# Kernel tuning notes

Hardware: AMD Instinct MI355X
Metric: run time of the kernel (lower is better)

Reference implementation:

```python
import jax, jax.numpy as jnp
import numpy as np

N = 50000      # nodes
E = 200000     # edges
IN = 768       # in_dim
HID = 256      # hidden_dim
OUT = 64       # out_dim
H = 4          # heads in conv1
R = 6          # n_relations
NEG = 0.2      # LeakyReLU negative slope (PyG default)
EPS = 1e-5     # LayerNorm eps


def layer_norm(h, g, b):
    mu = jnp.mean(h, axis=-1, keepdims=True)
    var = jnp.mean((h - mu) ** 2, axis=-1, keepdims=True)
    return (h - mu) * jax.lax.rsqrt(var + EPS) * g + b


def gat_layer(x, src, dst, W, a_src, a_dst, bias, heads, dh):
    # project: [N, heads, dh]
    h = (x @ W).reshape(-1, heads, dh)
    # per-node attention logits [N, heads]
    al_s = jnp.sum(h * a_src, axis=-1)
    al_d = jnp.sum(h * a_dst, axis=-1)
    # per-edge scores (edge j->i: source contributes al_s[j], target al_d[i])
    e = jax.nn.leaky_relu(al_s[src] + al_d[dst], NEG)  # [E, heads]
    # segment softmax over edges sharing the same destination node
    e_max = jax.ops.segment_max(e, dst, num_segments=N)        # [N, heads]
    ex = jnp.exp(e - e_max[dst])                               # [E, heads]
    denom = jax.ops.segment_sum(ex, dst, num_segments=N)       # [N, heads]
    alpha = ex / denom[dst]                                    # [E, heads]
    # weighted scatter-aggregate of source messages
    msg = h[src] * alpha[:, :, None]                            # [E, heads, dh]
    out = jax.ops.segment_sum(msg, dst, num_segments=N)        # [N, heads, dh]
    return out.reshape(-1, heads * dh) + bias


def setup_inputs() -> dict:
    key = jax.random.key(0)
    ks = jax.random.split(key, 16)
    s = 0.05  # keep attention logits tame
    return {
        "x": jax.random.normal(ks[0], (N, IN), jnp.float32),
        "edge_index": jax.random.randint(ks[1], (2, E), 0, N, dtype=jnp.int64),
        "edge_type": jax.random.randint(ks[2], (E,), 0, R, dtype=jnp.int64),
        "edge_emb": jax.random.normal(ks[3], (R, IN), jnp.float32) * s,
        "W1": jax.random.normal(ks[4], (IN, H * (HID // H)), jnp.float32) * s,
        "a_src1": jax.random.normal(ks[5], (H, HID // H), jnp.float32) * s,
        "a_dst1": jax.random.normal(ks[6], (H, HID // H), jnp.float32) * s,
        "b1": jnp.zeros((HID,), jnp.float32),
        "g1": jnp.ones((HID,), jnp.float32),
        "be1": jnp.zeros((HID,), jnp.float32),
        "W2": jax.random.normal(ks[7], (HID, OUT), jnp.float32) * s,
        "a_src2": jax.random.normal(ks[8], (1, OUT), jnp.float32) * s,
        "a_dst2": jax.random.normal(ks[9], (1, OUT), jnp.float32) * s,
        "b2": jnp.zeros((OUT,), jnp.float32),
        "g2": jnp.ones((OUT,), jnp.float32),
        "be2": jnp.zeros((OUT,), jnp.float32),
    }


def reference(x, edge_index, edge_type, edge_emb, W1, a_src1, a_dst1, b1, g1, be1,
              W2, a_src2, a_dst2, b2, g2, be2):
    src, dst = edge_index[0], edge_index[1]
    edge_feat = edge_emb[edge_type]                 # [E, IN]
    x_mod = x.at[src].set(x[src] + edge_feat)
    h = gat_layer(x_mod, src, dst, W1, a_src1, a_dst1, b1, H, HID // H)
    h = layer_norm(h, g1, be1)
    h = jax.nn.elu(h)                                # dropout off (inference)
    h = gat_layer(h, src, dst, W2, a_src2, a_dst2, b2, 1, OUT)
    h = layer_norm(h, g2, be2)
    return h
```

## Files before the change

### kernel.cpp

```cpp
#include <hip/hip_runtime.h>
#include <cstdint>
#include <cstddef>

#define NN 50000
#define NE 200000
#define IND 768
#define HID 256
#define OUTD 64
#define NB 196

typedef __bf16 bf16;
typedef __bf16 bf16x8 __attribute__((ext_vector_type(8)));
typedef float f32x4 __attribute__((ext_vector_type(4)));

__global__ __launch_bounds__(256) void k_edge_prep(const int* __restrict__ ei,
                                                   int* __restrict__ le, int* __restrict__ deg) {
  int e = blockIdx.x * 256 + threadIdx.x;
  if (e < NE) {
    atomicMax(&le[ei[e]], e);
    atomicAdd(&deg[ei[NE + e]], 1);
  }
}

__global__ __launch_bounds__(256) void k_scan_block(const int* __restrict__ deg,
                                                    int* __restrict__ excl, int* __restrict__ bsum) {
  __shared__ int sm[256];
  int tid = threadIdx.x;
  int i = blockIdx.x * 256 + tid;
  int v = (i < NN) ? deg[i] : 0;
  sm[tid] = v;
  __syncthreads();
#pragma unroll
  for (int off = 1; off < 256; off <<= 1) {
    int t = (tid >= off) ? sm[tid - off] : 0;
    __syncthreads();
    sm[tid] += t;
    __syncthreads();
  }
  if (i < NN) excl[i] = sm[tid] - v;
  if (tid == 255) bsum[blockIdx.x] = sm[255];
}

__global__ __launch_bounds__(256) void k_scan_partials(const int* __restrict__ bsum,
                                                       int* __restrict__ bbase) {
  __shared__ int sm[256];
  int tid = threadIdx.x;
  int v = (tid < NB) ? bsum[tid] : 0;
  sm[tid] = v;
  __syncthreads();
#pragma unroll
  for (int off = 1; off < 256; off <<= 1) {
    int t = (tid >= off) ? sm[tid - off] : 0;
    __syncthreads();
    sm[tid] += t;
    __syncthreads();
  }
  bbase[tid] = sm[tid] - v;
}

__global__ __launch_bounds__(256) void k_add_base(const int* __restrict__ excl,
                                                  const int* __restrict__ bbase,
                                                  int* __restrict__ rowstart, int* __restrict__ cur) {
  int i = blockIdx.x * 256 + threadIdx.x;
  if (i < NN) {
    int rs = excl[i] + bbase[i >> 8];
    rowstart[i] = rs;
    cur[i] = rs;
  }
}

__global__ __launch_bounds__(256) void k_scatter_csr(const int* __restrict__ ei,
                                                     int* __restrict__ cur, int* __restrict__ csr) {
  int e = blockIdx.x * 256 + threadIdx.x;
  if (e < NE) {
    int d = ei[NE + e];
    int pos = atomicAdd(&cur[d], 1);
    csr[pos] = ei[e];
  }
}

__global__ __launch_bounds__(256) void k_transpose(const float* __restrict__ W,
                                                   bf16* __restrict__ Wt, int K, int NC) {
  int k = blockIdx.x * 256 + threadIdx.x;
  int n = blockIdx.y;
  if (k < K) Wt[n * K + k] = (bf16)W[k * NC + n];
}

template <typename OutT, bool FUSE>
__global__ __launch_bounds__(256) void k_gemm_bt(const bf16* __restrict__ A,
                                                 const float* __restrict__ Ax,
                                                 const int* __restrict__ le,
                                                 const int* __restrict__ et,
                                                 const float* __restrict__ eemb,
                                                 const bf16* __restrict__ Bt,
                                                 OutT* __restrict__ C,
                                                 int M, int K, int NC,
                                                 const float* __restrict__ aS,
                                                 const float* __restrict__ aD,
                                                 float* __restrict__ alS,
                                                 float* __restrict__ alD,
                                                 int alStride) {
  __shared__ bf16 As[128 * 32];
  __shared__ bf16 Bs[128 * 32];
  const int tid = threadIdx.x;
  const int lane = tid & 63;
  const int wave = tid >> 6;
  const int wr = wave >> 1, wc = wave & 1;
  const int ln15 = lane & 15, q = lane >> 4;
  const int n0 = blockIdx.x * 128;
  const int m0 = blockIdx.y * 128;
  const int r0 = tid >> 2;
  const int ce = (tid & 3) << 3;

  const int rA1 = min(m0 + r0, M - 1);
  const int rA2 = min(m0 + 64 + r0, M - 1);
  const int rB1 = min(n0 + r0, NC - 1);
  const int rB2 = min(n0 + 64 + r0, NC - 1);

  int e1 = -1, e2 = -1;
  if (FUSE) {
    int l1 = le[rA1]; if (l1 >= 0) e1 = et[l1];
    int l2 = le[rA2]; if (l2 >= 0) e2 = et[l2];
  }

  f32x4 acc[4][4] = {};

  for (int kt = 0; kt < K; kt += 32) {
    bf16x8 va, vb;
    int4 va_i, vb_i;
    if (FUSE) {
      const float* p1 = Ax + (size_t)rA1 * K + kt + ce;
      const float* p2 = Ax + (size_t)rA2 * K + kt + ce;
      float4 a0 = *(const float4*)p1, a1 = *(const float4*)(p1 + 4);
      float4 b0 = *(const float4*)p2, b1 = *(const float4*)(p2 + 4);
      if (e1 >= 0) {
        const float* q1 = eemb + (size_t)e1 * K + kt + ce;
        float4 t0 = *(const float4*)q1, t1 = *(const float4*)(q1 + 4);
        a0.x += t0.x; a0.y += t0.y; a0.z += t0.z; a0.w += t0.w;
        a1.x += t1.x; a1.y += t1.y; a1.z += t1.z; a1.w += t1.w;
      }
      if (e2 >= 0) {
        const float* q2 = eemb + (size_t)e2 * K + kt + ce;
        float4 t0 = *(const float4*)q2, t1 = *(const float4*)(q2 + 4);
        b0.x += t0.x; b0.y += t0.y; b0.z += t0.z; b0.w += t0.w;
        b1.x += t1.x; b1.y += t1.y; b1.z += t1.z; b1.w += t1.w;
      }
      va[0] = (bf16)a0.x; va[1] = (bf16)a0.y; va[2] = (bf16)a0.z; va[3] = (bf16)a0.w;
      va[4] = (bf16)a1.x; va[5] = (bf16)a1.y; va[6] = (bf16)a1.z; va[7] = (bf16)a1.w;
      vb[0] = (bf16)b0.x; vb[1] = (bf16)b0.y; vb[2] = (bf16)b0.z; vb[3] = (bf16)b0.w;
      vb[4] = (bf16)b1.x; vb[5] = (bf16)b1.y; vb[6] = (bf16)b1.z; vb[7] = (bf16)b1.w;
    } else {
      va_i = *(const int4*)(A + (size_t)rA1 * K + kt + ce);
      vb_i = *(const int4*)(A + (size_t)rA2 * K + kt + ce);
    }
    int4 wb1 = *(const int4*)(Bt + (size_t)rB1 * K + kt + ce);
    int4 wb2 = *(const int4*)(Bt + (size_t)rB2 * K + kt + ce);
    __syncthreads();
    if (FUSE) {
      *(bf16x8*)(As + r0 * 32 + ce) = va;
      *(bf16x8*)(As + (64 + r0) * 32 + ce) = vb;
    } else {
      *(int4*)(As + r0 * 32 + ce) = va_i;
      *(int4*)(As + (64 + r0) * 32 + ce) = vb_i;
    }
    *(int4*)(Bs + r0 * 32 + ce) = wb1;
    *(int4*)(Bs + (64 + r0) * 32 + ce) = wb2;
    __syncthreads();
    bf16x8 af[4], bfr[4];
#pragma unroll
    for (int i = 0; i < 4; i++)
      af[i] = *(const bf16x8*)(As + (wr * 64 + i * 16 + ln15) * 32 + q * 8);
#pragma unroll
    for (int i = 0; i < 4; i++)
      bfr[i] = *(const bf16x8*)(Bs + (wc * 64 + i * 16 + ln15) * 32 + q * 8);
#pragma unroll
    for (int mi = 0; mi < 4; mi++)
#pragma unroll
      for (int ni = 0; ni < 4; ni++)
        acc[mi][ni] = __builtin_amdgcn_mfma_f32_16x16x32_bf16(af[mi], bfr[ni], acc[mi][ni], 0, 0, 0);
  }

#pragma unroll
  for (int mi = 0; mi < 4; mi++)
#pragma unroll
    for (int ni = 0; ni < 4; ni++)
#pragma unroll
      for (int r = 0; r < 4; r++) {
        int row = m0 + wr * 64 + mi * 16 + q * 4 + r;
        int col = n0 + wc * 64 + ni * 16 + ln15;
        if (row < M && col < NC) C[(size_t)row * NC + col] = (OutT)acc[mi][ni][r];
      }

  if (n0 + wc * 64 < NC) {
    const int hd = (n0 + wc * 64) >> 6;
#pragma unroll
    for (int mi = 0; mi < 4; mi++)
#pragma unroll
      for (int r = 0; r < 4; r++) {
        float ps = 0.f, pd = 0.f;
#pragma unroll
        for (int ni = 0; ni < 4; ni++) {
          int col = n0 + wc * 64 + ni * 16 + ln15;
          float w_s = (col < NC) ? aS[col] : 0.f;
          float w_d = (col < NC) ? aD[col] : 0.f;
          ps += acc[mi][ni][r] * w_s;
          pd += acc[mi][ni][r] * w_d;
        }
#pragma unroll
        for (int off = 1; off < 16; off <<= 1) {
          ps += __shfl_xor(ps, off);
          pd += __shfl_xor(pd, off);
        }
        int row = m0 + wr * 64 + mi * 16 + q * 4 + r;
        if (ln15 == 0 && row < M) {
          alS[row * alStride + hd] = ps;
          alD[row * alStride + hd] = pd;
        }
      }
  }
}

__global__ __launch_bounds__(256) void k_agg_ln1(const int* __restrict__ rowstart,
                                                 const int* __restrict__ deg,
                                                 const int* __restrict__ csr,
                                                 const bf16* __restrict__ h1,
                                                 const float* __restrict__ alS,
                                                 const float* __restrict__ alD,
                                                 const float* __restrict__ b1,
                                                 const float* __restrict__ g1,
                                                 const float* __restrict__ be1,
                                                 bf16* __restrict__ hln) {
  __shared__ float red[8];
  int n = blockIdx.x, f = threadIdx.x, hd = f >> 6;
  int start = rowstart[n], cnt = deg[n];
  float ald = alD[n * 4 + hd];
  float accv = 0.f, accw = 0.f;
  for (int j = 0; j < cnt; j++) {
    int s = csr[start + j];
    float logit = alS[s * 4 + hd] + ald;
    logit = logit >= 0.f ? logit : 0.2f * logit;
    float w = __expf(logit);
    accv += w * (float)h1[(size_t)s * HID + f];
    accw += w;
  }
  float v = (cnt > 0) ? accv / accw : 0.f;
  v += b1[f];
  float s = v, ss = v * v;
#pragma unroll
  for (int off = 32; off; off >>= 1) { s += __shfl_xor(s, off); ss += __shfl_xor(ss, off); }
  if ((f & 63) == 0) { red[f >> 6] = s; red[4 + (f >> 6)] = ss; }
  __syncthreads();
  float tot = red[0] + red[1] + red[2] + red[3];
  float tss = red[4] + red[5] + red[6] + red[7];
  float mu = tot * (1.f / HID);
  float var = tss * (1.f / HID) - mu * mu;
  float y = (v - mu) * rsqrtf(var + 1e-5f) * g1[f] + be1[f];
  y = y > 0.f ? y : __expf(y) - 1.f;
  hln[(size_t)n * HID + f] = (bf16)y;
}

__global__ __launch_bounds__(64) void k_agg_ln2(const int* __restrict__ rowstart,
                                                const int* __restrict__ deg,
                                                const int* __restrict__ csr,
                                                const float* __restrict__ h2,
                                                const float* __restrict__ alS,
                                                const float* __restrict__ alD,
                                                const float* __restrict__ b2,
                                                const float* __restrict__ g2,
                                                const float* __restrict__ be2,
                                                float* __restrict__ out) {
  int n = blockIdx.x, f = threadIdx.x;
  int start = rowstart[n], cnt = deg[n];
  float ald = alD[n];
  float accv = 0.f, accw = 0.f;
  for (int j = 0; j < cnt; j++) {
    int s = csr[start + j];
    float logit = alS[s] + ald;
    logit = logit >= 0.f ? logit : 0.2f * logit;
    float w = __expf(logit);
    accv += w * h2[(size_t)s * OUTD + f];
    accw += w;
  }
  float v = (cnt > 0) ? accv / accw : 0.f;
  v += b2[f];
  float s = v, ss = v * v;
#pragma unroll
  for (int off = 32; off; off >>= 1) { s += __shfl_xor(s, off); ss += __shfl_xor(ss, off); }
  float mu = s * (1.f / OUTD);
  float var = ss * (1.f / OUTD) - mu * mu;
  out[(size_t)n * OUTD + f] = (v - mu) * rsqrtf(var + 1e-5f) * g2[f] + be2[f];
}

extern "C" void kernel_launch(void* const* d_in, const int* in_sizes, int n_in,
                              void* d_out, int out_size, void* d_ws, size_t ws_size,
                              hipStream_t stream) {
  const float* x    = (const float*)d_in[0];
  const int*   ei   = (const int*)d_in[1];
  const int*   et   = (const int*)d_in[2];
  const float* eemb = (const float*)d_in[3];
  const float* W1   = (const float*)d_in[4];
  const float* as1  = (const float*)d_in[5];
  const float* ad1  = (const float*)d_in[6];
  const float* b1   = (const float*)d_in[7];
  const float* g1   = (const float*)d_in[8];
  const float* be1  = (const float*)d_in[9];
  const float* W2   = (const float*)d_in[10];
  const float* as2  = (const float*)d_in[11];
  const float* ad2  = (const float*)d_in[12];
  const float* b2   = (const float*)d_in[13];
  const float* g2   = (const float*)d_in[14];
  const float* be2  = (const float*)d_in[15];
  float* out = (float*)d_out;

  char* base = (char*)d_ws;
  size_t off = 0;
  auto alloc = [&](size_t bytes) -> void* {
    void* p = base + off;
    off = (off + bytes + 255) & ~(size_t)255;
    return p;
  };
  int*   le    = (int*)alloc((size_t)NN * 4);
  int*   deg   = (int*)alloc((size_t)NN * 4);
  int*   excl  = (int*)alloc((size_t)NN * 4);
  int*   bsum  = (int*)alloc(256 * 4);
  int*   bbase = (int*)alloc(256 * 4);
  int*   rowst = (int*)alloc((size_t)NN * 4);
  int*   cur   = (int*)alloc((size_t)NN * 4);
  int*   csr   = (int*)alloc((size_t)NE * 4);
  bf16*  h1    = (bf16*)alloc((size_t)NN * HID * 2);
  float* alS1  = (float*)alloc((size_t)NN * 4 * 4);
  float* alD1  = (float*)alloc((size_t)NN * 4 * 4);
  bf16*  hln   = (bf16*)alloc((size_t)NN * HID * 2);
  float* h2    = (float*)alloc((size_t)NN * OUTD * 4);
  float* alS2  = (float*)alloc((size_t)NN * 4);
  float* alD2  = (float*)alloc((size_t)NN * 4);
  bf16*  W1t   = (bf16*)alloc((size_t)HID * IND * 2);
  bf16*  W2t   = (bf16*)alloc((size_t)OUTD * HID * 2);

  hipMemsetAsync(le, 0xFF, (size_t)NN * 4, stream);
  hipMemsetAsync(deg, 0, (size_t)NN * 4, stream);

  k_edge_prep<<<(NE + 255) / 256, 256, 0, stream>>>(ei, le, deg);
  k_scan_block<<<NB, 256, 0, stream>>>(deg, excl, bsum);
  k_scan_partials<<<1, 256, 0, stream>>>(bsum, bbase);
  k_add_base<<<NB, 256, 0, stream>>>(excl, bbase, rowst, cur);
  k_scatter_csr<<<(NE + 255) / 256, 256, 0, stream>>>(ei, cur, csr);

  k_transpose<<<dim3(3, HID), 256, 0, stream>>>(W1, W1t, IND, HID);
  k_transpose<<<dim3(1, OUTD), 256, 0, stream>>>(W2, W2t, HID, OUTD);

  k_gemm_bt<bf16, true><<<dim3(2, (NN + 127) / 128), 256, 0, stream>>>(
      nullptr, x, le, et, eemb, W1t, h1, NN, IND, HID, as1, ad1, alS1, alD1, 4);
  k_agg_ln1<<<NN, 256, 0, stream>>>(rowst, deg, csr, h1, alS1, alD1, b1, g1, be1, hln);

  k_gemm_bt<float, false><<<dim3(1, (NN + 127) / 128), 256, 0, stream>>>(
      hln, nullptr, nullptr, nullptr, nullptr, W2t, h2, NN, HID, OUTD, as2, ad2, alS2, alD2, 1);
  k_agg_ln2<<<NN, 64, 0, stream>>>(rowst, deg, csr, h2, alS2, alD2, b2, g2, be2, out);
}
```

Measured before the change: 484.9 us.

## Double-buffer GEMM LDS tiles with padding and branchless edge-embedding add

The GEMM main loop becomes a two-stage software pipeline: global loads for the next K tile are issued before the MFMA compute on the current LDS buffer, and only one barrier is taken per iteration. LDS rows are padded from 32 to 40 elements to cut bank conflicts on the fragment reads. The edge-type embedding add no longer branches: a zero row is appended to the embedding table so untouched nodes read zeros. In exchange the kernel uses twice the LDS, holds more live registers, and launches one extra small kernel.

```diff
diff --git a/kernel.cpp b/kernel.cpp
--- a/kernel.cpp
+++ b/kernel.cpp
@@ -20,6 +20,12 @@
     atomicMax(&le[ei[e]], e);
     atomicAdd(&deg[ei[NE + e]], 1);
   }
+}
+
+__global__ __launch_bounds__(256) void k_eembz(const float* __restrict__ eemb,
+                                               float* __restrict__ ez) {
+  int i = blockIdx.x * 256 + threadIdx.x;
+  if (i < 7 * IND) ez[i] = (i < 6 * IND) ? eemb[i] : 0.f;
 }
 
 __global__ __launch_bounds__(256) void k_scan_block(const int* __restrict__ deg,
@@ -91,7 +97,7 @@
                                                  const float* __restrict__ Ax,
                                                  const int* __restrict__ le,
                                                  const int* __restrict__ et,
-                                                 const float* __restrict__ eemb,
+                                                 const float* __restrict__ eembz,
                                                  const bf16* __restrict__ Bt,
                                                  OutT* __restrict__ C,
                                                  int M, int K, int NC,
@@ -100,8 +106,9 @@
                                                  float* __restrict__ alS,
                                                  float* __restrict__ alD,
                                                  int alStride) {
-  __shared__ bf16 As[128 * 32];
-  __shared__ bf16 Bs[128 * 32];
+  constexpr int PAD = 40;
+  __shared__ bf16 As[2][128 * PAD];
+  __shared__ bf16 Bs[2][128 * PAD];
   const int tid = threadIdx.x;
   const int lane = tid & 63;
   const int wave = tid >> 6;
@@ -117,68 +124,97 @@
   const int rB1 = min(n0 + r0, NC - 1);
   const int rB2 = min(n0 + 64 + r0, NC - 1);
 
-  int e1 = -1, e2 = -1;
-  if (FUSE) {
-    int l1 = le[rA1]; if (l1 >= 0) e1 = et[l1];
-    int l2 = le[rA2]; if (l2 >= 0) e2 = et[l2];
-  }
+  const float* pA1 = nullptr; const float* pA2 = nullptr;
+  const float* pE1 = nullptr; const float* pE2 = nullptr;
+  const bf16* pAb1 = nullptr; const bf16* pAb2 = nullptr;
+  if constexpr (FUSE) {
+    int l1 = le[rA1]; int e1 = (l1 >= 0) ? et[l1] : 6;
+    int l2 = le[rA2]; int e2 = (l2 >= 0) ? et[l2] : 6;
+    pA1 = Ax + (size_t)rA1 * K + ce;
+    pA2 = Ax + (size_t)rA2 * K + ce;
+    pE1 = eembz + (size_t)e1 * K + ce;
+    pE2 = eembz + (size_t)e2 * K + ce;
+  } else {
+    pAb1 = A + (size_t)rA1 * K + ce;
+    pAb2 = A + (size_t)rA2 * K + ce;
+  }
+  const bf16* pB1 = Bt + (size_t)rB1 * K + ce;
+  const bf16* pB2 = Bt + (size_t)rB2 * K + ce;
+
+  float4 a0, a1, b0, b1, t0, t1, t2, t3;
+  int4 va_i, vb_i, wb1, wb2;
+
+  auto issue = [&](int kt) {
+    if constexpr (FUSE) {
+      a0 = *(const float4*)(pA1 + kt);
+      a1 = *(const float4*)(pA1 + kt + 4);
+      b0 = *(const float4*)(pA2 + kt);
+      b1 = *(const float4*)(pA2 + kt + 4);
+      t0 = *(const float4*)(pE1 + kt);
+      t1 = *(const float4*)(pE1 + kt + 4);
+      t2 = *(const float4*)(pE2 + kt);
+      t3 = *(const float4*)(pE2 + kt + 4);
+    } else {
+      va_i = *(const int4*)(pAb1 + kt);
+      vb_i = *(const int4*)(pAb2 + kt);
+    }
+    wb1 = *(const int4*)(pB1 + kt);
+    wb2 = *(const int4*)(pB2 + kt);
+  };
+
+  auto commit = [&](int buf) {
+    if constexpr (FUSE) {
+      bf16x8 va, vb;
+      va[0] = (bf16)(a0.x + t0.x); va[1] = (bf16)(a0.y + t0.y);
+      va[2] = (bf16)(a0.z + t0.z); va[3] = (bf16)(a0.w + t0.w);
+      va[4] = (bf16)(a1.x + t1.x); va[5] = (bf16)(a1.y + t1.y);
+      va[6] = (bf16)(a1.z + t1.z); va[7] = (bf16)(a1.w + t1.w);
+      vb[0] = (bf16)(b0.x + t2.x); vb[1] = (bf16)(b0.y + t2.y);
+      vb[2] = (bf16)(b0.z + t2.z); vb[3] = (bf16)(b0.w + t2.w);
+      vb[4] = (bf16)(b1.x + t3.x); vb[5] = (bf16)(b1.y + t3.y);
+      vb[6] = (bf16)(b1.z + t3.z); vb[7] = (bf16)(b1.w + t3.w);
+      *(bf16x8*)(&As[buf][r0 * PAD + ce]) = va;
+      *(bf16x8*)(&As[buf][(64 + r0) * PAD + ce]) = vb;
+    } else {
+      *(int4*)(&As[buf][r0 * PAD + ce]) = va_i;
+      *(int4*)(&As[buf][(64 + r0) * PAD + ce]) = vb_i;
+    }
+    *(int4*)(&Bs[buf][r0 * PAD + ce]) = wb1;
+    *(int4*)(&Bs[buf][(64 + r0) * PAD + ce]) = wb2;
+  };
 
   f32x4 acc[4][4] = {};
 
-  for (int kt = 0; kt < K; kt += 32) {
-    bf16x8 va, vb;
-    int4 va_i, vb_i;
-    if (FUSE) {
-      const float* p1 = Ax + (size_t)rA1 * K + kt + ce;
-      const float* p2 = Ax + (size_t)rA2 * K + kt + ce;
-      float4 a0 = *(const float4*)p1, a1 = *(const float4*)(p1 + 4);
-      float4 b0 = *(const float4*)p2, b1 = *(const float4*)(p2 + 4);
-      if (e1 >= 0) {
-        const float* q1 = eemb + (size_t)e1 * K + kt + ce;
-        float4 t0 = *(const float4*)q1, t1 = *(const float4*)(q1 + 4);
-        a0.x += t0.x; a0.y += t0.y; a0.z += t0.z; a0.w += t0.w;
-        a1.x += t1.x; a1.y += t1.y; a1.z += t1.z; a1.w += t1.w;
-      }
-      if (e2 >= 0) {
-        const float* q2 = eemb + (size_t)e2 * K + kt + ce;
-        float4 t0 = *(const float4*)q2, t1 = *(const float4*)(q2 + 4);
-        b0.x += t0.x; b0.y += t0.y; b0.z += t0.z; b0.w += t0.w;
-        b1.x += t1.x; b1.y += t1.y; b1.z += t1.z; b1.w += t1.w;
-      }
-      va[0] = (bf16)a0.x; va[1] = (bf16)a0.y; va[2] = (bf16)a0.z; va[3] = (bf16)a0.w;
-      va[4] = (bf16)a1.x; va[5] = (bf16)a1.y; va[6] = (bf16)a1.z; va[7] = (bf16)a1.w;
-      vb[0] = (bf16)b0.x; vb[1] = (bf16)b0.y; vb[2] = (bf16)b0.z; vb[3] = (bf16)b0.w;
-      vb[4] = (bf16)b1.x; vb[5] = (bf16)b1.y; vb[6] = (bf16)b1.z; vb[7] = (bf16)b1.w;
-    } else {
-      va_i = *(const int4*)(A + (size_t)rA1 * K + kt + ce);
-      vb_i = *(const int4*)(A + (size_t)rA2 * K + kt + ce);
-    }
-    int4 wb1 = *(const int4*)(Bt + (size_t)rB1 * K + kt + ce);
-    int4 wb2 = *(const int4*)(Bt + (size_t)rB2 * K + kt + ce);
-    __syncthreads();
-    if (FUSE) {
-      *(bf16x8*)(As + r0 * 32 + ce) = va;
-      *(bf16x8*)(As + (64 + r0) * 32 + ce) = vb;
-    } else {
-      *(int4*)(As + r0 * 32 + ce) = va_i;
-      *(int4*)(As + (64 + r0) * 32 + ce) = vb_i;
-    }
-    *(int4*)(Bs + r0 * 32 + ce) = wb1;
-    *(int4*)(Bs + (64 + r0) * 32 + ce) = wb2;
-    __syncthreads();
+  auto compute = [&](int buf) {
     bf16x8 af[4], bfr[4];
 #pragma unroll
     for (int i = 0; i < 4; i++)
-      af[i] = *(const bf16x8*)(As + (wr * 64 + i * 16 + ln15) * 32 + q * 8);
+      af[i] = *(const bf16x8*)(&As[buf][(wr * 64 + i * 16 + ln15) * PAD + q * 8]);
 #pragma unroll
     for (int i = 0; i < 4; i++)
-      bfr[i] = *(const bf16x8*)(Bs + (wc * 64 + i * 16 + ln15) * 32 + q * 8);
+      bfr[i] = *(const bf16x8*)(&Bs[buf][(wc * 64 + i * 16 + ln15) * PAD + q * 8]);
 #pragma unroll
     for (int mi = 0; mi < 4; mi++)
 #pragma unroll
       for (int ni = 0; ni < 4; ni++)
         acc[mi][ni] = __builtin_amdgcn_mfma_f32_16x16x32_bf16(af[mi], bfr[ni], acc[mi][ni], 0, 0, 0);
-  }
+  };
+
+  const int NT = K >> 5;
+
+  issue(0);
+  commit(0);
+  __syncthreads();
+
+  int cur = 0;
+  for (int t = 0; t < NT - 1; ++t) {
+    issue((t + 1) << 5);
+    compute(cur);
+    commit(cur ^ 1);
+    __syncthreads();
+    cur ^= 1;
+  }
+  compute(cur);
 
 #pragma unroll
   for (int mi = 0; mi < 4; mi++)
@@ -336,11 +372,13 @@
   float* alD2  = (float*)alloc((size_t)NN * 4);
   bf16*  W1t   = (bf16*)alloc((size_t)HID * IND * 2);
   bf16*  W2t   = (bf16*)alloc((size_t)OUTD * HID * 2);
+  float* eembz = (float*)alloc((size_t)7 * IND * 4);
 
   hipMemsetAsync(le, 0xFF, (size_t)NN * 4, stream);
   hipMemsetAsync(deg, 0, (size_t)NN * 4, stream);
 
   k_edge_prep<<<(NE + 255) / 256, 256, 0, stream>>>(ei, le, deg);
+  k_eembz<<<(7 * IND + 255) / 256, 256, 0, stream>>>(eemb, eembz);
   k_scan_block<<<NB, 256, 0, stream>>>(deg, excl, bsum);
   k_scan_partials<<<1, 256, 0, stream>>>(bsum, bbase);
   k_add_base<<<NB, 256, 0, stream>>>(excl, bbase, rowst, cur);
@@ -350,7 +388,7 @@
   k_transpose<<<dim3(1, OUTD), 256, 0, stream>>>(W2, W2t, HID, OUTD);
 
   k_gemm_bt<bf16, true><<<dim3(2, (NN + 127) / 128), 256, 0, stream>>>(
-      nullptr, x, le, et, eemb, W1t, h1, NN, IND, HID, as1, ad1, alS1, alD1, 4);
+      nullptr, x, le, et, eembz, W1t, h1, NN, IND, HID, as1, ad1, alS1, alD1, 4);
   k_agg_ln1<<<NN, 256, 0, stream>>>(rowst, deg, csr, h1, alS1, alD1, b1, g1, be1, hln);
 
   k_gemm_bt<float, false><<<dim3(1, (NN + 127) / 128), 256, 0, stream>>>(
```

Measured after the change: 470.3 us. -3.0%, faster.

## Pre-convert x+edge embedding to bf16 and stage GEMM tiles via global_load_lds

Applied to the files above, without the earlier changes.

Adds a separate pass that adds the edge-type embedding (selected by last-writing edge) to x and writes a bf16 copy of the first-layer input. The GEMM then loads A and B tiles straight into LDS with the global_load_lds builtin, instead of going through registers. This removes the fp32 loads and conversion from the GEMM inner loop and avoids reading the fp32 x twice across the two column blocks. The cost is an extra pass that writes and rereads a 77MB bf16 buffer, plus a second barrier per k-step because there is no double buffering. The workspace is reorganised so the new buffer aliases hln, h2 and the layer-2 logits.

```diff
diff --git a/kernel.cpp b/kernel.cpp
--- a/kernel.cpp
+++ b/kernel.cpp
@@ -20,6 +20,35 @@
     atomicMax(&le[ei[e]], e);
     atomicAdd(&deg[ei[NE + e]], 1);
   }
+}
+
+__global__ __launch_bounds__(256) void k_eembz(const float* __restrict__ eemb,
+                                               float* __restrict__ ez) {
+  int i = blockIdx.x * 256 + threadIdx.x;
+  if (i < 7 * IND) ez[i] = (i < 6 * IND) ? eemb[i] : 0.f;
+}
+
+__global__ __launch_bounds__(256) void k_prep_a(const float* __restrict__ x,
+                                                const int* __restrict__ le,
+                                                const int* __restrict__ et,
+                                                const float* __restrict__ eembz,
+                                                bf16* __restrict__ A1) {
+  int idx = blockIdx.x * 256 + threadIdx.x;
+  if (idx >= NN * (IND / 8)) return;
+  int row = idx / (IND / 8);
+  int c = (idx - row * (IND / 8)) * 8;
+  int l = le[row];
+  int e = (l >= 0) ? et[l] : 6;
+  const float* px = x + (size_t)row * IND + c;
+  const float* pe = eembz + (size_t)e * IND + c;
+  float4 v0 = *(const float4*)px, v1 = *(const float4*)(px + 4);
+  float4 e0 = *(const float4*)pe, e1 = *(const float4*)(pe + 4);
+  bf16x8 o;
+  o[0] = (bf16)(v0.x + e0.x); o[1] = (bf16)(v0.y + e0.y);
+  o[2] = (bf16)(v0.z + e0.z); o[3] = (bf16)(v0.w + e0.w);
+  o[4] = (bf16)(v1.x + e1.x); o[5] = (bf16)(v1.y + e1.y);
+  o[6] = (bf16)(v1.z + e1.z); o[7] = (bf16)(v1.w + e1.w);
+  *(bf16x8*)(A1 + (size_t)row * IND + c) = o;
 }
 
 __global__ __launch_bounds__(256) void k_scan_block(const int* __restrict__ deg,
@@ -86,12 +115,13 @@
   if (k < K) Wt[n * K + k] = (bf16)W[k * NC + n];
 }
 
-template <typename OutT, bool FUSE>
+__device__ __forceinline__ void gld16(const bf16* g, bf16* l) {
+  __builtin_amdgcn_global_load_lds((const __attribute__((address_space(1))) void*)g,
+                                   (__attribute__((address_space(3))) void*)l, 16, 0, 0);
+}
+
+template <typename OutT>
 __global__ __launch_bounds__(256) void k_gemm_bt(const bf16* __restrict__ A,
-                                                 const float* __restrict__ Ax,
-                                                 const int* __restrict__ le,
-                                                 const int* __restrict__ et,
-                                                 const float* __restrict__ eemb,
                                                  const bf16* __restrict__ Bt,
                                                  OutT* __restrict__ C,
                                                  int M, int K, int NC,
@@ -109,62 +139,25 @@
   const int ln15 = lane & 15, q = lane >> 4;
   const int n0 = blockIdx.x * 128;
   const int m0 = blockIdx.y * 128;
-  const int r0 = tid >> 2;
-  const int ce = (tid & 3) << 3;
-
-  const int rA1 = min(m0 + r0, M - 1);
-  const int rA2 = min(m0 + 64 + r0, M - 1);
-  const int rB1 = min(n0 + r0, NC - 1);
-  const int rB2 = min(n0 + 64 + r0, NC - 1);
-
-  int e1 = -1, e2 = -1;
-  if (FUSE) {
-    int l1 = le[rA1]; if (l1 >= 0) e1 = et[l1];
-    int l2 = le[rA2]; if (l2 >= 0) e2 = et[l2];
-  }
+
+  const int sr = lane >> 2;
+  const int scol = (lane & 3) * 8;
+  const int gA0 = min(m0 + wave * 32 + sr, M - 1);
+  const int gA1 = min(m0 + wave * 32 + 16 + sr, M - 1);
+  const int gB0 = min(n0 + wave * 32 + sr, NC - 1);
+  const int gB1 = min(n0 + wave * 32 + 16 + sr, NC - 1);
+  bf16* lA0 = As + (wave * 32) * 32;
+  bf16* lA1 = As + (wave * 32 + 16) * 32;
+  bf16* lB0 = Bs + (wave * 32) * 32;
+  bf16* lB1 = Bs + (wave * 32 + 16) * 32;
 
   f32x4 acc[4][4] = {};
 
   for (int kt = 0; kt < K; kt += 32) {
-    bf16x8 va, vb;
-    int4 va_i, vb_i;
-    if (FUSE) {
-      const float* p1 = Ax + (size_t)rA1 * K + kt + ce;
-      const float* p2 = Ax + (size_t)rA2 * K + kt + ce;
-      float4 a0 = *(const float4*)p1, a1 = *(const float4*)(p1 + 4);
-      float4 b0 = *(const float4*)p2, b1 = *(const float4*)(p2 + 4);
-      if (e1 >= 0) {
-        const float* q1 = eemb + (size_t)e1 * K + kt + ce;
-        float4 t0 = *(const float4*)q1, t1 = *(const float4*)(q1 + 4);
-        a0.x += t0.x; a0.y += t0.y; a0.z += t0.z; a0.w += t0.w;
-        a1.x += t1.x; a1.y += t1.y; a1.z += t1.z; a1.w += t1.w;
-      }
-      if (e2 >= 0) {
-        const float* q2 = eemb + (size_t)e2 * K + kt + ce;
-        float4 t0 = *(const float4*)q2, t1 = *(const float4*)(q2 + 4);
-        b0.x += t0.x; b0.y += t0.y; b0.z += t0.z; b0.w += t0.w;
-        b1.x += t1.x; b1.y += t1.y; b1.z += t1.z; b1.w += t1.w;
-      }
-      va[0] = (bf16)a0.x; va[1] = (bf16)a0.y; va[2] = (bf16)a0.z; va[3] = (bf16)a0.w;
-      va[4] = (bf16)a1.x; va[5] = (bf16)a1.y; va[6] = (bf16)a1.z; va[7] = (bf16)a1.w;
-      vb[0] = (bf16)b0.x; vb[1] = (bf16)b0.y; vb[2] = (bf16)b0.z; vb[3] = (bf16)b0.w;
-      vb[4] = (bf16)b1.x; vb[5] = (bf16)b1.y; vb[6] = (bf16)b1.z; vb[7] = (bf16)b1.w;
-    } else {
-      va_i = *(const int4*)(A + (size_t)rA1 * K + kt + ce);
-      vb_i = *(const int4*)(A + (size_t)rA2 * K + kt + ce);
-    }
-    int4 wb1 = *(const int4*)(Bt + (size_t)rB1 * K + kt + ce);
-    int4 wb2 = *(const int4*)(Bt + (size_t)rB2 * K + kt + ce);
-    __syncthreads();
-    if (FUSE) {
-      *(bf16x8*)(As + r0 * 32 + ce) = va;
-      *(bf16x8*)(As + (64 + r0) * 32 + ce) = vb;
-    } else {
-      *(int4*)(As + r0 * 32 + ce) = va_i;
-      *(int4*)(As + (64 + r0) * 32 + ce) = vb_i;
-    }
-    *(int4*)(Bs + r0 * 32 + ce) = wb1;
-    *(int4*)(Bs + (64 + r0) * 32 + ce) = wb2;
+    gld16(A + (size_t)gA0 * K + kt + scol, lA0);
+    gld16(A + (size_t)gA1 * K + kt + scol, lA1);
+    gld16(Bt + (size_t)gB0 * K + kt + scol, lB0);
+    gld16(Bt + (size_t)gB1 * K + kt + scol, lB1);
     __syncthreads();
     bf16x8 af[4], bfr[4];
 #pragma unroll
@@ -178,6 +171,7 @@
 #pragma unroll
       for (int ni = 0; ni < 4; ni++)
         acc[mi][ni] = __builtin_amdgcn_mfma_f32_16x16x32_bf16(af[mi], bfr[ni], acc[mi][ni], 0, 0, 0);
+    __syncthreads();
   }
 
 #pragma unroll
@@ -330,17 +324,22 @@
   bf16*  h1    = (bf16*)alloc((size_t)NN * HID * 2);
   float* alS1  = (float*)alloc((size_t)NN * 4 * 4);
   float* alD1  = (float*)alloc((size_t)NN * 4 * 4);
-  bf16*  hln   = (bf16*)alloc((size_t)NN * HID * 2);
-  float* h2    = (float*)alloc((size_t)NN * OUTD * 4);
-  float* alS2  = (float*)alloc((size_t)NN * 4);
-  float* alD2  = (float*)alloc((size_t)NN * 4);
   bf16*  W1t   = (bf16*)alloc((size_t)HID * IND * 2);
   bf16*  W2t   = (bf16*)alloc((size_t)OUTD * HID * 2);
+  float* eembz = (float*)alloc((size_t)7 * IND * 4);
+  char*  R     = (char*)alloc((size_t)NN * IND * 2);
+  bf16*  A1    = (bf16*)R;
+  bf16*  hln   = (bf16*)R;
+  float* h2    = (float*)(R + (size_t)NN * HID * 2);
+  float* alS2  = (float*)(R + (size_t)NN * HID * 2 + (size_t)NN * OUTD * 4);
+  float* alD2  = (float*)(R + (size_t)NN * HID * 2 + (size_t)NN * OUTD * 4 + (size_t)NN * 4);
 
   hipMemsetAsync(le, 0xFF, (size_t)NN * 4, stream);
   hipMemsetAsync(deg, 0, (size_t)NN * 4, stream);
 
   k_edge_prep<<<(NE + 255) / 256, 256, 0, stream>>>(ei, le, deg);
+  k_eembz<<<(7 * IND + 255) / 256, 256, 0, stream>>>(eemb, eembz);
+  k_prep_a<<<(NN * (IND / 8) + 255) / 256, 256, 0, stream>>>(x, le, et, eembz, A1);
   k_scan_block<<<NB, 256, 0, stream>>>(deg, excl, bsum);
   k_scan_partials<<<1, 256, 0, stream>>>(bsum, bbase);
   k_add_base<<<NB, 256, 0, stream>>>(excl, bbase, rowst, cur);
@@ -349,11 +348,11 @@
   k_transpose<<<dim3(3, HID), 256, 0, stream>>>(W1, W1t, IND, HID);
   k_transpose<<<dim3(1, OUTD), 256, 0, stream>>>(W2, W2t, HID, OUTD);
 
-  k_gemm_bt<bf16, true><<<dim3(2, (NN + 127) / 128), 256, 0, stream>>>(
-      nullptr, x, le, et, eemb, W1t, h1, NN, IND, HID, as1, ad1, alS1, alD1, 4);
+  k_gemm_bt<bf16><<<dim3(2, (NN + 127) / 128), 256, 0, stream>>>(
+      A1, W1t, h1, NN, IND, HID, as1, ad1, alS1, alD1, 4);
   k_agg_ln1<<<NN, 256, 0, stream>>>(rowst, deg, csr, h1, alS1, alD1, b1, g1, be1, hln);
 
-  k_gemm_bt<float, false><<<dim3(1, (NN + 127) / 128), 256, 0, stream>>>(
-      hln, nullptr, nullptr, nullptr, nullptr, W2t, h2, NN, HID, OUTD, as2, ad2, alS2, alD2, 1);
+  k_gemm_bt<float><<<dim3(1, (NN + 127) / 128), 256, 0, stream>>>(
+      hln, W2t, h2, NN, HID, OUTD, as2, ad2, alS2, alD2, 1);
   k_agg_ln2<<<NN, 64, 0, stream>>>(rowst, deg, csr, h2, alS2, alD2, b2, g2, be2, out);
 }
```

After: 481.1 us. About the same (-0.8%).
